# Kernel optimization log

Measured on AMD Instinct MI355X. Metric: run time of the kernel, lower is better.

## Reference

```python
import jax, jax.numpy as jnp
import numpy as np

B, C, H, W, D, V = 1, 32, 128, 160, 48, 3


def _make_proj_matrices():
    # K @ [R|t] per view, small rotations/baselines so warps land mostly in-bounds
    K = np.array([[400.0, 0.0, 80.0], [0.0, 400.0, 64.0], [0.0, 0.0, 1.0]])
    mats = []
    for v in range(V):
        a = 0.04 * v
        R = np.array([[np.cos(a), 0.0, np.sin(a)], [0.0, 1.0, 0.0], [-np.sin(a), 0.0, np.cos(a)]])
        t = np.array([120.0 * v, 0.0, 0.0])  # baseline in mm, consistent with depth ~425..935
        P = np.eye(4)
        P[:3, :3] = K @ R
        P[:3, 3] = K @ t
        mats.append(P)
    return jnp.asarray(np.stack(mats)[None], dtype=jnp.float32)  # [1,V,4,4]


def setup_inputs() -> dict:
    key = jax.random.key(0)
    k0, k1, k2, kw = jax.random.split(key, 4)
    feat0 = jax.random.normal(k0, (B, C, H, W), jnp.float32)
    feat1 = jax.random.normal(k1, (B, C, H, W), jnp.float32)
    feat2 = jax.random.normal(k2, (B, C, H, W), jnp.float32)
    depth_values = jnp.broadcast_to(
        jnp.linspace(425.0, 935.0, D, dtype=jnp.float32)[None], (B, D))
    w_reg = jax.random.normal(kw, (1, C, 3, 3, 3), jnp.float32) * 0.05
    b_reg = jnp.zeros((1,), jnp.float32)
    return dict(feat0=feat0, feat1=feat1, feat2=feat2,
                proj_matrices=_make_proj_matrices(),
                depth_values=depth_values, w_reg=w_reg, b_reg=b_reg,
                num_depth=D)


def _bilinear_sample(fea, gx, gy):
    # fea: [C,H,W]; gx,gy: [N] pixel coords (align_corners=True convention),
    # zero padding outside image (matches F.grid_sample padding_mode='zeros').
    h, w = fea.shape[1], fea.shape[2]
    x0 = jnp.floor(gx)
    y0 = jnp.floor(gy)
    wx = gx - x0
    wy = gy - y0

    def corner(xi, yi, wgt):
        valid = ((xi >= 0) & (xi <= w - 1) & (yi >= 0) & (yi <= h - 1)).astype(fea.dtype)
        xc = jnp.clip(xi, 0, w - 1).astype(jnp.int32)
        yc = jnp.clip(yi, 0, h - 1).astype(jnp.int32)
        return fea[:, yc, xc] * (wgt * valid)[None]  # [C,N]

    return (corner(x0, y0, (1 - wx) * (1 - wy)) +
            corner(x0 + 1, y0, wx * (1 - wy)) +
            corner(x0, y0 + 1, (1 - wx) * wy) +
            corner(x0 + 1, y0 + 1, wx * wy))


def homo_warping(src_fea, src_proj, ref_proj, depth_values):
    # src_fea [B,C,H,W], projs [B,4,4], depth_values [B,D] -> [B,C,D,H,W]
    b, c, h, w = src_fea.shape
    d = depth_values.shape[1]
    proj = src_proj @ jnp.linalg.inv(ref_proj)
    rot = proj[:, :3, :3]           # [B,3,3]
    trans = proj[:, :3, 3]          # [B,3]
    yy, xx = jnp.meshgrid(jnp.arange(h, dtype=src_fea.dtype),
                          jnp.arange(w, dtype=src_fea.dtype), indexing='ij')
    xyz = jnp.stack([xx.ravel(), yy.ravel(), jnp.ones(h * w, src_fea.dtype)], 0)  # [3,HW]
    rot_xyz = jnp.einsum('bij,jn->bin', rot, xyz)                                  # [B,3,HW]
    p = rot_xyz[:, :, None, :] * depth_values[:, None, :, None] + trans[:, :, None, None]  # [B,3,D,HW]
    z = p[:, 2]
    gx = (p[:, 0] / z).reshape(b, -1)  # [B, D*HW]
    gy = (p[:, 1] / z).reshape(b, -1)
    warped = jax.vmap(_bilinear_sample)(src_fea, gx, gy)  # [B,C,D*HW]
    return warped.reshape(b, c, d, h, w)


def reference(feat0, feat1, feat2, proj_matrices, depth_values, w_reg, b_reg, num_depth):
    features = [feat0, feat1, feat2]
    projs = [proj_matrices[:, v] for v in range(proj_matrices.shape[1])]
    ref_fea, ref_proj = features[0], projs[0]
    num_views = len(features)
    b, c, h, w = ref_fea.shape

    ref_volume = jnp.broadcast_to(ref_fea[:, :, None], (b, c, num_depth, h, w))
    volume_sum = ref_volume
    volume_sq_sum = ref_volume ** 2
    for src_fea, src_proj in zip(features[1:], projs[1:]):
        wv = homo_warping(src_fea, src_proj, ref_proj, depth_values)
        volume_sum = volume_sum + wv
        volume_sq_sum = volume_sq_sum + wv * wv

    volume_variance = volume_sq_sum / num_views - (volume_sum / num_views) ** 2

    # cost_regularization stand-in: 3D conv C -> 1, SAME padding, then squeeze channel
    cost = jax.lax.conv_general_dilated(
        volume_variance, w_reg, window_strides=(1, 1, 1), padding='SAME',
        dimension_numbers=('NCDHW', 'OIDHW', 'NCDHW'))
    cost = cost[:, 0] + b_reg[0]            # [B,D,H,W]

    prob_volume = jax.nn.softmax(cost, axis=1)
    depth = jnp.sum(prob_volume * depth_values[:, :, None, None], axis=1)  # [B,H,W]
    photometric_confidence = jnp.max(prob_volume, axis=1)                   # [B,H,W]
    return depth, photometric_confidence
```

## Files before the change

kernel.cpp:

```cpp
#include <hip/hip_runtime.h>
#include <hip/hip_fp16.h>
#include <math.h>

#define Cc 32
#define Hc 128
#define Wc 160
#define Dc 48
#define HWc (Hc*Wc)
#define TSX 16
#define TSY 8
#define HALOX (TSX+2)
#define HALOY (TSY+2)
#define NPOS (HALOX*HALOY)
#define DCHUNK 6
#define NCHUNK (Dc/DCHUNK)
#define NPASS 3
#define NSLOT (DCHUNK+2)


typedef _Float16 h8v __attribute__((ext_vector_type(8)));
typedef float f32x4 __attribute__((ext_vector_type(4)));

union F4H { float4 f; __half2 h[4]; };
union PackCW { __half2 h[4]; float4 f; };
union AF { float4 f; h8v h; };

__global__ void k_pre(const float* __restrict__ f0, const float* __restrict__ f1,
                      const float* __restrict__ f2, const float* __restrict__ proj,
                      const float* __restrict__ wreg,
                      _Float16* __restrict__ o0, _Float16* __restrict__ o1, _Float16* __restrict__ o2,
                      float* __restrict__ wsproj, _Float16* __restrict__ w2h) {
    const int tid = threadIdx.x;
    const int pxl = tid & 127, h = tid >> 7;
    const int p = blockIdx.x * 128 + pxl;
    {
        const float* f = (blockIdx.y == 0) ? f0 : (blockIdx.y == 1) ? f1 : f2;
        _Float16*    o = (blockIdx.y == 0) ? o0 : (blockIdx.y == 1) ? o1 : o2;
        float v[16];
#pragma unroll
        for (int c = 0; c < 16; c++) v[c] = f[(h * 16 + c) * HWc + p];
        union { __half2 hh[8]; float4 f4[2]; } rec;
#pragma unroll
        for (int c = 0; c < 8; c++) rec.hh[c] = __floats2half2_rn(v[2 * c], v[2 * c + 1]);
        float4* o4 = (float4*)(o + (size_t)p * Cc);
        o4[h * 2 + 0] = rec.f4[0];
        o4[h * 2 + 1] = rec.f4[1];
    }
    if (blockIdx.x == 0 && blockIdx.y == 0) {
        for (int i = tid; i < 9 * 3 * Cc; i += 256) {
            int ch = i & 31;
            int t  = i >> 5;
            int kd = t % 3;
            int khkw = t / 3;
            w2h[i] = (_Float16)wreg[ch * 27 + kd * 9 + khkw];
        }
        if (tid == 0) {
            float a[4][8];
            for (int i = 0; i < 4; i++)
                for (int j = 0; j < 4; j++) {
                    a[i][j]     = proj[i * 4 + j];
                    a[i][j + 4] = (i == j) ? 1.f : 0.f;
                }
            for (int col = 0; col < 4; col++) {
                int piv = col; float best = fabsf(a[col][col]);
                for (int r = col + 1; r < 4; r++) {
                    float v = fabsf(a[r][col]);
                    if (v > best) { best = v; piv = r; }
                }
                if (piv != col)
                    for (int j = 0; j < 8; j++) { float t = a[col][j]; a[col][j] = a[piv][j]; a[piv][j] = t; }
                float inv = 1.f / a[col][col];
                for (int j = 0; j < 8; j++) a[col][j] *= inv;
                for (int r = 0; r < 4; r++) if (r != col) {
                    float f = a[r][col];
                    for (int j = 0; j < 8; j++) a[r][j] -= f * a[col][j];
                }
            }
            for (int v = 1; v < 3; v++) {
                const float* P = proj + v * 16;
                float M[3][4];
                for (int i = 0; i < 3; i++)
                    for (int j = 0; j < 4; j++) {
                        float s = 0.f;
                        for (int k = 0; k < 4; k++) s += P[i * 4 + k] * a[k][4 + j];
                        M[i][j] = s;
                    }
                float* o = wsproj + (v - 1) * 12;
                o[0] = M[0][0]; o[1] = M[0][1]; o[2] = M[0][2];
                o[3] = M[1][0]; o[4] = M[1][1]; o[5] = M[1][2];
                o[6] = M[2][0]; o[7] = M[2][1]; o[8] = M[2][2];
                o[9] = M[0][3]; o[10] = M[1][3]; o[11] = M[2][3];
            }
        }
    }
}

__global__ __launch_bounds__(256, 4) void k_cost(
    const _Float16* __restrict__ fT0, const _Float16* __restrict__ fT1,
    const _Float16* __restrict__ fT2, const float* __restrict__ dvals,
    const float4* __restrict__ w2h4, const float* __restrict__ wsproj,
    float* __restrict__ costvol, float* __restrict__ bnd)
{
    __shared__ float4 varA[NPOS * 4];
    __shared__ float4 varB[NPOS * 4];
    __shared__ float4 parW[NPOS];
    __shared__ uint2  parIc[NPOS];
    __shared__ float4 cost_l4[NSLOT * 32];
    __shared__ float projl[24];
    float* cost_l = (float*)cost_l4;

    const int tid = threadIdx.x;
    if (tid < 24) projl[tid] = wsproj[tid];
#pragma unroll
    for (int i = 0; i < 4; i++) cost_l[i * 256 + tid] = 0.f;
    __syncthreads();

    const int tileX = blockIdx.x;
    const int sy    = blockIdx.y;
    const int zc    = blockIdx.z;
    const int d0    = zc * DCHUNK;
    const int baseH = sy * TSY - 1, baseW = tileX * TSX - 1;

    const int posq = tid >> 2;
    const int cc   = tid & 3;

    const int wid  = tid >> 6;
    const int lane = tid & 63;
    const int lrow = lane & 15;
    const int lsel = lane >> 4;

    const float4* fT0_4 = (const float4*)fT0;
    const float4* fT1_4 = (const float4*)fT1;
    const float4* fT2_4 = (const float4*)fT2;

    h8v bfr[9];
    {
        const int kdc = (lrow < 3) ? lrow : 0;
#pragma unroll
        for (int t = 0; t < 9; t++) {
            AF u; u.f = w2h4[(t * 3 + kdc) * 4 + lsel];
            bfr[t] = u.h;
        }
    }

    float rAx[2], rAy[2], rAz[2];
    float trn[2][3];
#pragma unroll
    for (int v = 0; v < 2; v++) {
        trn[v][0] = projl[v * 12 + 9];
        trn[v][1] = projl[v * 12 + 10];
        trn[v][2] = projl[v * 12 + 11];
    }
    bool aok;
    {
        int pp = (tid < NPOS) ? tid : 0;
        int py = pp / HALOX, px = pp % HALOX;
        int hyi = baseH + py, hxi = baseW + px;
        aok = (tid < NPOS) && hyi >= 0 && hyi < Hc && hxi >= 0 && hxi < Wc;
        float hx = (float)hxi, hy = (float)hyi;
#pragma unroll
        for (int v = 0; v < 2; v++) {
            const float* R = projl + v * 12;
            rAx[v] = fmaf(R[0], hx, fmaf(R[1], hy, R[2]));
            rAy[v] = fmaf(R[3], hx, fmaf(R[4], hy, R[5]));
            rAz[v] = fmaf(R[6], hx, fmaf(R[7], hy, R[8]));
        }
    }

    int    bmask = 0;
    float4 rfv[NPASS];
#pragma unroll
    for (int s = 0; s < NPASS; s++) {
        int p = posq + s * 64;
        bool act = p < NPOS;
        int pp = act ? p : 0;
        int py = pp / HALOX, px = pp % HALOX;
        int hyi = baseH + py, hxi = baseW + px;
        bool ok = act && hyi >= 0 && hyi < Hc && hxi >= 0 && hxi < Wc;
        if (ok) bmask |= (1 << s);
        rfv[s] = ok ? fT0_4[(hyi * Wc + hxi) * 4 + cc] : make_float4(0.f, 0.f, 0.f, 0.f);
    }

    auto phaseA = [&](int dpn) {
        const float depthN = dvals[dpn];
        if (aok) {
            float cw[2][4]; unsigned int pkc[2];
#pragma unroll
            for (int v = 0; v < 2; v++) {
                float X = fmaf(rAx[v], depthN, trn[v][0]);
                float Y = fmaf(rAy[v], depthN, trn[v][1]);
                float Z = fmaf(rAz[v], depthN, trn[v][2]);
                float iz = 1.f / Z;
                float gx = X * iz, gy = Y * iz;
                float x0f = floorf(gx), y0f = floorf(gy);
                float wx = gx - x0f, wy = gy - y0f;
                int x0 = (int)x0f, y0 = (int)y0f;
                bool vx0 = (x0 >= 0) & (x0 <= Wc - 1);
                bool vx1 = (x0 + 1 >= 0) & (x0 + 1 <= Wc - 1);
                bool vy0 = (y0 >= 0) & (y0 <= Hc - 1);
                bool vy1 = (y0 + 1 >= 0) & (y0 + 1 <= Hc - 1);
                unsigned int xc0 = (unsigned int)min(max(x0, 0), Wc - 1);
                unsigned int xc1 = (unsigned int)min(max(x0 + 1, 0), Wc - 1);
                unsigned int yc0 = (unsigned int)min(max(y0, 0), Hc - 1);
                unsigned int yc1 = (unsigned int)min(max(y0 + 1, 0), Hc - 1);
                float ax = 1.f - wx, ay = 1.f - wy;
                cw[v][0] = (vx0 && vy0) ? ax * ay : 0.f;
                cw[v][1] = (vx1 && vy0) ? wx * ay : 0.f;
                cw[v][2] = (vx0 && vy1) ? ax * wy : 0.f;
                cw[v][3] = (vx1 && vy1) ? wx * wy : 0.f;
                pkc[v] = xc0 | (xc1 << 8) | (yc0 << 16) | (yc1 << 24);
            }
            PackCW pc;
            pc.h[0] = __floats2half2_rn(cw[0][0], cw[0][1]);
            pc.h[1] = __floats2half2_rn(cw[0][2], cw[0][3]);
            pc.h[2] = __floats2half2_rn(cw[1][0], cw[1][1]);
            pc.h[3] = __floats2half2_rn(cw[1][2], cw[1][3]);
            parW[tid] = pc.f;
            parIc[tid] = make_uint2(pkc[0], pkc[1]);
        }
    };

    const __half2 kT3 = __float2half2_rn(1.f / 3.f);
    const __half2 kN9 = __float2half2_rn(-1.f / 9.f);

    auto phaseB = [&](float4* dst) {
#pragma unroll
        for (int s = 0; s < NPASS; s++) {
            int p = posq + s * 64;
            if (p >= NPOS) continue;
            const int vaddr = (p << 2) + (cc ^ ((p >> 1) & 3));
            if (!((bmask >> s) & 1)) {
                dst[vaddr] = make_float4(0.f, 0.f, 0.f, 0.f);
                continue;
            }
            PackCW pc; pc.f = parW[p];
            uint2 pi = parIc[p];
            __half2 c0a = __low2half2(pc.h[0]), c0b = __high2half2(pc.h[0]);
            __half2 c0c = __low2half2(pc.h[1]), c0d = __high2half2(pc.h[1]);
            __half2 c1a = __low2half2(pc.h[2]), c1b = __high2half2(pc.h[2]);
            __half2 c1c = __low2half2(pc.h[3]), c1d = __high2half2(pc.h[3]);
            unsigned int a = pi.x, b = pi.y;
            int x00 = a & 0xff, x01 = (a >> 8) & 0xff, y00 = (a >> 16) & 0xff, y01 = a >> 24;
            int x10 = b & 0xff, x11 = (b >> 8) & 0xff, y10 = (b >> 16) & 0xff, y11 = b >> 24;
            int i00 = y00 * Wc + x00, i01 = y00 * Wc + x01;
            int i02 = y01 * Wc + x00, i03 = y01 * Wc + x01;
            int i10 = y10 * Wc + x10, i11 = y10 * Wc + x11;
            int i12 = y11 * Wc + x10, i13 = y11 * Wc + x11;
            F4H rf; rf.f = rfv[s];
            F4H t00, t01, t10, t11, u00v, u01v, u10v, u11v, vo;
            t00.f = fT1_4[i00 * 4 + cc];
            t01.f = fT1_4[i01 * 4 + cc];
            t10.f = fT1_4[i02 * 4 + cc];
            t11.f = fT1_4[i03 * 4 + cc];
            u00v.f = fT2_4[i10 * 4 + cc];
            u01v.f = fT2_4[i11 * 4 + cc];
            u10v.f = fT2_4[i12 * 4 + cc];
            u11v.f = fT2_4[i13 * 4 + cc];
#pragma unroll
            for (int j = 0; j < 4; j++) {
                __half2 a1 = __hfma2(c0a, t00.h[j], __hfma2(c0b, t01.h[j],
                             __hfma2(c0c, t10.h[j], __hmul2(c0d, t11.h[j]))));
                __half2 a2 = __hfma2(c1a, u00v.h[j], __hfma2(c1b, u01v.h[j],
                             __hfma2(c1c, u10v.h[j], __hmul2(c1d, u11v.h[j]))));
                __half2 r  = rf.h[j];
                __half2 sm = __hadd2(r, __hadd2(a1, a2));
                __half2 sq = __hfma2(r, r, __hfma2(a1, a1, __hmul2(a2, a2)));
                vo.h[j] = __hfma2(__hmul2(sm, sm), kN9, __hmul2(sq, kT3));
            }
            dst[vaddr] = vo.f;
        }
    };

    auto conv = [&](const float4* src, int dp) {
#pragma unroll
        for (int g = 0; g < 2; g++) {
            const int R = (wid << 1) + g;
            f32x4 acc = {0.f, 0.f, 0.f, 0.f};
#pragma unroll
            for (int t = 0; t < 9; t++) {
                const int dy = t / 3, dx = t % 3;
                const int pos = (R + dy) * HALOX + dx + lrow;
                AF a; a.f = src[(pos << 2) + (lsel ^ ((pos >> 1) & 3))];
                acc = __builtin_amdgcn_mfma_f32_16x16x32_f16(a.h, bfr[t], acc, 0, 0, 0);
            }
            if (lrow < 3) {
                const int idx = ((dp - d0) + 2 - lrow) * 32 + R * 4 + lsel;
                float4 c = cost_l4[idx];
                c.x += acc[0]; c.y += acc[1]; c.z += acc[2]; c.w += acc[3];
                cost_l4[idx] = c;
            }
        }
    };

    const int dpLast = d0 + DCHUNK - 1;

    phaseA(d0);
    __syncthreads();
    phaseB(varA);
    __syncthreads();
    phaseA(d0 + 1);
    __syncthreads();

    for (int i = 0; i < DCHUNK / 2; i++) {
        const int t = d0 + 2 * i;
        phaseB(varB);
        conv(varA, t);
        __syncthreads();
        if (t + 2 <= dpLast) {
            phaseA(t + 2);
            __syncthreads();
        }
        if (t + 2 <= dpLast) phaseB(varA);
        conv(varB, t + 1);
        __syncthreads();
        if (t + 3 <= dpLast) {
            phaseA(t + 3);
            __syncthreads();
        }
    }

    const int c    = tid & 127;
    const int half = tid >> 7;
    const int gy = sy * TSY + (c >> 4), gx = tileX * TSX + (c & 15);
    const int gpx = gy * Wc + gx;
#pragma unroll
    for (int k = 0; k < 4; k++) {
        const int slot = half * 4 + k;
        const float v = cost_l[slot * 128 + c];
        if (slot == 0) {
            if (zc > 0) bnd[(zc * 2 + 0) * HWc + gpx] = v;
        } else if (slot == NSLOT - 1) {
            if (zc < NCHUNK - 1) bnd[(zc * 2 + 1) * HWc + gpx] = v;
        } else {
            costvol[(size_t)(d0 + slot - 1) * HWc + gpx] = v;
        }
    }
}

__global__ void k_softmax(const float* __restrict__ costvol, const float* __restrict__ bnd,
                          const float* __restrict__ dvals,
                          const float* __restrict__ breg, float* __restrict__ out)
{
    __shared__ float sm[4][64], ss[4][64], sd[4][64], sx[4][64];
    const int tid = threadIdx.x;
    const int pxl = tid & 63, g = tid >> 6;
    const int px = blockIdx.x * 64 + pxl;
    const float bias = breg[0];

    float c[12];
    float m = -1e30f;
#pragma unroll
    for (int i = 0; i < 12; i++) {
        const int d = g * 12 + i;
        float v = costvol[(size_t)d * HWc + px] + bias;
        if (i == 0) { if (g > 0) v += bnd[(4 * g - 1) * HWc + px]; }
        if (i == 6) v += bnd[(4 * g + 1) * HWc + px];
        if (i == 5) v += bnd[(4 * g + 2) * HWc + px];
        if (i == 11) { if (g < 3) v += bnd[(4 * g + 4) * HWc + px]; }
        c[i] = v;
        m = fmaxf(m, v);
    }
    float se = 0.f, sed = 0.f, me = 0.f;
#pragma unroll
    for (int i = 0; i < 12; i++) {
        float e = __expf(c[i] - m);
        se += e;
        sed = fmaf(e, dvals[g * 12 + i], sed);
        me = fmaxf(me, e);
    }
    sm[g][pxl] = m; ss[g][pxl] = se; sd[g][pxl] = sed; sx[g][pxl] = me;
    __syncthreads();
    if (g == 0) {
        float M = fmaxf(fmaxf(sm[0][pxl], sm[1][pxl]), fmaxf(sm[2][pxl], sm[3][pxl]));
        float SE = 0.f, SD = 0.f, ME = 0.f;
#pragma unroll
        for (int j = 0; j < 4; j++) {
            float w = __expf(sm[j][pxl] - M);
            SE += ss[j][pxl] * w;
            SD += sd[j][pxl] * w;
            ME = fmaxf(ME, sx[j][pxl] * w);
        }
        float inv = 1.f / SE;
        out[px]       = SD * inv;
        out[HWc + px] = ME * inv;
    }
}

extern "C" void kernel_launch(void* const* d_in, const int* in_sizes, int n_in,
                              void* d_out, int out_size, void* d_ws, size_t ws_size,
                              hipStream_t stream) {
    const float* f0    = (const float*)d_in[0];
    const float* f1    = (const float*)d_in[1];
    const float* f2    = (const float*)d_in[2];
    const float* proj  = (const float*)d_in[3];
    const float* dvals = (const float*)d_in[4];
    const float* wreg  = (const float*)d_in[5];
    const float* breg  = (const float*)d_in[6];

    float* ws      = (float*)d_ws;
    float* wsproj  = ws;
    _Float16* w2h  = (_Float16*)(ws + 32);
    _Float16* fT0h = (_Float16*)(ws + 32 + 432);
    _Float16* fT1h = fT0h + (size_t)HWc * Cc;
    _Float16* fT2h = fT1h + (size_t)HWc * Cc;
    float* costvol = (float*)(fT2h + (size_t)HWc * Cc);
    float* bnd     = costvol + (size_t)Dc * HWc;

    k_pre<<<dim3(HWc / 128, 3), 256, 0, stream>>>(f0, f1, f2, proj, wreg,
                                                  fT0h, fT1h, fT2h, wsproj, w2h);

    dim3 grid(Wc / TSX, Hc / TSY, NCHUNK);
    k_cost<<<grid, 256, 0, stream>>>(fT0h, fT1h, fT2h, dvals, (const float4*)w2h,
                                     wsproj, costvol, bnd);

    k_softmax<<<HWc / 64, 256, 0, stream>>>(costvol, bnd, dvals, breg, (float*)d_out);
}
```

Baseline: 119.2 us.

## Double-buffer warp parameters and enlarge depth chunk to cut barriers

Raises the depth chunk per block from 6 to 8, so there are fewer z-blocks and less halo-boundary recomputation. The per-pixel sampling parameters get two shared buffers (A/B), which lets the next depth's parameter computation overlap with the current gather and conv. Each depth step now needs one barrier instead of two. In exchange, shared memory use per block rises, which can lower occupancy, and the grid has fewer blocks for parallelism. The softmax boundary indexing is rewritten to match the new chunking.

```diff
diff --git a/kernel.cpp b/kernel.cpp
--- a/kernel.cpp
+++ b/kernel.cpp
@@ -12,7 +12,7 @@
 #define HALOX (TSX+2)
 #define HALOY (TSY+2)
 #define NPOS (HALOX*HALOY)
-#define DCHUNK 6
+#define DCHUNK 8
 #define NCHUNK (Dc/DCHUNK)
 #define NPASS 3
 #define NSLOT (DCHUNK+2)
@@ -103,8 +103,10 @@
 {
     __shared__ float4 varA[NPOS * 4];
     __shared__ float4 varB[NPOS * 4];
-    __shared__ float4 parW[NPOS];
-    __shared__ uint2  parIc[NPOS];
+    __shared__ float4 parWA[NPOS];
+    __shared__ float4 parWB[NPOS];
+    __shared__ uint2  parIA[NPOS];
+    __shared__ uint2  parIB[NPOS];
     __shared__ float4 cost_l4[NSLOT * 32];
     __shared__ float projl[24];
     float* cost_l = (float*)cost_l4;
@@ -112,7 +114,7 @@
     const int tid = threadIdx.x;
     if (tid < 24) projl[tid] = wsproj[tid];
 #pragma unroll
-    for (int i = 0; i < 4; i++) cost_l[i * 256 + tid] = 0.f;
+    for (int i = 0; i < 5; i++) cost_l[i * 256 + tid] = 0.f;
     __syncthreads();
 
     const int tileX = blockIdx.x;
@@ -181,7 +183,7 @@
         rfv[s] = ok ? fT0_4[(hyi * Wc + hxi) * 4 + cc] : make_float4(0.f, 0.f, 0.f, 0.f);
     }
 
-    auto phaseA = [&](int dpn) {
+    auto phaseA = [&](int dpn, float4* pW, uint2* pI) {
         const float depthN = dvals[dpn];
         if (aok) {
             float cw[2][4]; unsigned int pkc[2];
@@ -215,15 +217,15 @@
             pc.h[1] = __floats2half2_rn(cw[0][2], cw[0][3]);
             pc.h[2] = __floats2half2_rn(cw[1][0], cw[1][1]);
             pc.h[3] = __floats2half2_rn(cw[1][2], cw[1][3]);
-            parW[tid] = pc.f;
-            parIc[tid] = make_uint2(pkc[0], pkc[1]);
+            pW[tid] = pc.f;
+            pI[tid] = make_uint2(pkc[0], pkc[1]);
         }
     };
 
     const __half2 kT3 = __float2half2_rn(1.f / 3.f);
     const __half2 kN9 = __float2half2_rn(-1.f / 9.f);
 
-    auto phaseB = [&](float4* dst) {
+    auto phaseB = [&](const float4* pW, const uint2* pI, float4* dst) {
 #pragma unroll
         for (int s = 0; s < NPASS; s++) {
             int p = posq + s * 64;
@@ -233,8 +235,8 @@
                 dst[vaddr] = make_float4(0.f, 0.f, 0.f, 0.f);
                 continue;
             }
-            PackCW pc; pc.f = parW[p];
-            uint2 pi = parIc[p];
+            PackCW pc; pc.f = pW[p];
+            uint2 pi = pI[p];
             __half2 c0a = __low2half2(pc.h[0]), c0b = __high2half2(pc.h[0]);
             __half2 c0c = __low2half2(pc.h[1]), c0d = __high2half2(pc.h[1]);
             __half2 c1a = __low2half2(pc.h[2]), c1b = __high2half2(pc.h[2]);
@@ -294,29 +296,24 @@
 
     const int dpLast = d0 + DCHUNK - 1;
 
-    phaseA(d0);
+    phaseA(d0, parWA, parIA);
     __syncthreads();
-    phaseB(varA);
+    phaseB(parWA, parIA, varA);
+    phaseA(d0 + 1, parWB, parIB);
     __syncthreads();
-    phaseA(d0 + 1);
-    __syncthreads();
-
-    for (int i = 0; i < DCHUNK / 2; i++) {
-        const int t = d0 + 2 * i;
-        phaseB(varB);
-        conv(varA, t);
+
+    for (int i = 0; i < DCHUNK; i++) {
+        const int t = d0 + i;
+        if (i & 1) {
+            if (t + 1 <= dpLast) phaseB(parWA, parIA, varA);
+            conv(varB, t);
+            if (t + 2 <= dpLast) phaseA(t + 2, parWB, parIB);
+        } else {
+            if (t + 1 <= dpLast) phaseB(parWB, parIB, varB);
+            conv(varA, t);
+            if (t + 2 <= dpLast) phaseA(t + 2, parWA, parIA);
+        }
         __syncthreads();
-        if (t + 2 <= dpLast) {
-            phaseA(t + 2);
-            __syncthreads();
-        }
-        if (t + 2 <= dpLast) phaseB(varA);
-        conv(varB, t + 1);
-        __syncthreads();
-        if (t + 3 <= dpLast) {
-            phaseA(t + 3);
-            __syncthreads();
-        }
     }
 
     const int c    = tid & 127;
@@ -324,8 +321,8 @@
     const int gy = sy * TSY + (c >> 4), gx = tileX * TSX + (c & 15);
     const int gpx = gy * Wc + gx;
 #pragma unroll
-    for (int k = 0; k < 4; k++) {
-        const int slot = half * 4 + k;
+    for (int k = 0; k < 5; k++) {
+        const int slot = half * 5 + k;
         const float v = cost_l[slot * 128 + c];
         if (slot == 0) {
             if (zc > 0) bnd[(zc * 2 + 0) * HWc + gpx] = v;
@@ -353,10 +350,10 @@
     for (int i = 0; i < 12; i++) {
         const int d = g * 12 + i;
         float v = costvol[(size_t)d * HWc + px] + bias;
-        if (i == 0) { if (g > 0) v += bnd[(4 * g - 1) * HWc + px]; }
-        if (i == 6) v += bnd[(4 * g + 1) * HWc + px];
-        if (i == 5) v += bnd[(4 * g + 2) * HWc + px];
-        if (i == 11) { if (g < 3) v += bnd[(4 * g + 4) * HWc + px]; }
+        if ((d & 7) == 0 && d > 0)
+            v += bnd[(((d >> 3) - 1) * 2 + 1) * HWc + px];
+        if ((d & 7) == 7 && d < Dc - 1)
+            v += bnd[(((d >> 3) + 1) * 2 + 0) * HWc + px];
         c[i] = v;
         m = fmaxf(m, v);
     }
```

Result: slower. 152.2 us (+27.7%).
